# Kernel tuning notes

Hardware: AMD Instinct MI355X
Metric: run time of the kernel (lower is better)

The kernel has to match this reference:

```python
import jax, jax.numpy as jnp
import numpy as np

N = 50000          # num nodes
E = 600000         # num edges
F_IN = 128         # num_features
H = 128            # graph_hidden_dim
R = 2              # num_relations
L = 3              # n_layers_conv
BN_EPS = 1e-5
BN_BETA = 1e-4     # BatchNorm bias init per module code


def setup_inputs() -> dict:
    key = jax.random.key(0)
    ks = jax.random.split(key, 9)
    s_in = 1.0 / np.sqrt(F_IN)
    s_h = 1.0 / np.sqrt(H)
    return {
        "x": jax.random.normal(ks[0], (N, F_IN), jnp.float32),
        "edge_index": jax.random.randint(ks[1], (2, E), 0, N, jnp.int32),
        "edge_type": jax.random.randint(ks[2], (E,), 0, R, jnp.int32),
        "W0_rel": jax.random.normal(ks[3], (R, F_IN, H), jnp.float32) * s_in,
        "W0_root": jax.random.normal(ks[4], (F_IN, H), jnp.float32) * s_in,
        "b0": jnp.zeros((H,), jnp.float32),
        "Ws_rel": jax.random.normal(ks[5], (L, R, H, H), jnp.float32) * s_h,
        "Ws_root": jax.random.normal(ks[6], (L, H, H), jnp.float32) * s_h,
        "bs": jnp.zeros((L, H), jnp.float32),
    }


def batchnorm(x):
    # training-mode BatchNorm1d over nodes; weight=1, bias=1e-4 (per init)
    mu = jnp.mean(x, axis=0)
    var = jnp.mean((x - mu) ** 2, axis=0)  # biased var, as torch uses for norm
    return (x - mu) * jax.lax.rsqrt(var + BN_EPS) + BN_BETA


def rgcn_conv(x, src, dst, edge_type, W_rel, W_root, b):
    # PyG RGCNConv, aggr='mean': per-relation mean of x[src] at dst,
    # then per-relation linear, plus root transform and bias.
    seg = dst * R + edge_type  # combined (node, relation) segment id
    msgs = x[src]                                   # [E, d] gather
    sums = jax.ops.segment_sum(msgs, seg, num_segments=N * R)
    cnts = jax.ops.segment_sum(jnp.ones((src.shape[0],), x.dtype), seg,
                               num_segments=N * R)
    mean = sums.reshape(N, R, -1) / jnp.maximum(cnts, 1.0).reshape(N, R, 1)
    out = jnp.einsum('nrd,rdh->nh', mean, W_rel) + x @ W_root + b
    return out


def reference(x, edge_index, edge_type, W0_rel, W0_root, b0, Ws_rel, Ws_root, bs):
    src, dst = edge_index[0], edge_index[1]
    h = batchnorm(x)
    h = jax.nn.relu(rgcn_conv(h, src, dst, edge_type, W0_rel, W0_root, b0))
    for i in range(L):
        h_ = batchnorm(h)
        h_ = jax.nn.relu(rgcn_conv(h_, src, dst, edge_type,
                                   Ws_rel[i], Ws_root[i], bs[i]))
        h = h + h_  # conv_residual=True
    return h  # gconv_dropout == 0
```

## Files before the change

### kernel.cpp

```cpp
#include <hip/hip_runtime.h>
#include <hip/hip_bf16.h>

#define N_NODES 50000
#define N_EDGES 600000
#define F 128
#define R 2
#define NLAYER 4
#define NSEG (N_NODES * R)
#define SEGP (NSEG / 8)
#define NSCB 98
#define NB 384
#define BN_EPS 1e-5f
#define BETA 1e-4f

typedef __hip_bfloat16 bf16;
typedef __attribute__((ext_vector_type(8))) short short8;
typedef __attribute__((ext_vector_type(4))) float floatx4;

__global__ void k_wt(const float* __restrict__ W0_rel, const float* __restrict__ W0_root,
                     const float* __restrict__ Ws_rel, const float* __restrict__ Ws_root,
                     bf16* __restrict__ Bt) {
    int idx = blockIdx.x * 256 + threadIdx.x;
    if (idx >= NLAYER * NB * F) return;
    int l = idx / (NB * F);
    int rem = idx % (NB * F);
    int j = rem / F, d = rem % F;
    float v;
    if (j < 256) {
        int r = j >> 7, c = j & 127;
        v = (l == 0) ? W0_rel[(r * F + d) * F + c]
                     : Ws_rel[((size_t)((l - 1) * R + r) * F + d) * F + c];
    } else {
        int c = j - 256;
        v = (l == 0) ? W0_root[d * F + c]
                     : Ws_root[((size_t)(l - 1) * F + d) * F + c];
    }
    Bt[idx] = __float2bfloat16(v);
}

__global__ void k_count(const int* __restrict__ dst, const int* __restrict__ et,
                        int* __restrict__ cnt) {
    int g = blockIdx.x & 7;
    int lo = g * SEGP, hi = lo + SEGP;
    for (int e = (blockIdx.x >> 3) * 256 + threadIdx.x; e < N_EDGES; e += 65536) {
        int seg = dst[e] * R + et[e];
        if (seg >= lo && seg < hi) atomicAdd(&cnt[seg], 1);
    }
}

__global__ void k_scan1(const int* __restrict__ cnt, int* __restrict__ off,
                        int* __restrict__ bsum) {
    int t = threadIdx.x;
    int g = blockIdx.x * 1024 + t;
    int v = (g < NSEG) ? cnt[g] : 0;
    int lane = t & 63;
    int wv = t >> 6;
    int x = v;
    for (int d = 1; d < 64; d <<= 1) {
        int y = __shfl_up(x, d, 64);
        if (lane >= d) x += y;
    }
    __shared__ int wtot[16];
    if (lane == 63) wtot[wv] = x;
    __syncthreads();
    if (t < 16) {
        int s = wtot[t];
        for (int d = 1; d < 16; d <<= 1) {
            int y = __shfl_up(s, d, 64);
            if (t >= d) s += y;
        }
        wtot[t] = s;
    }
    __syncthreads();
    int wpre = (wv == 0) ? 0 : wtot[wv - 1];
    int incl = x + wpre;
    if (g < NSEG) off[g] = incl - v;
    if (t == 1023) bsum[blockIdx.x] = incl;
}

__global__ void k_scan2(int* __restrict__ bsum) {
    __shared__ int s[128];
    int t = threadIdx.x;
    int v = (t < NSCB) ? bsum[t] : 0;
    s[t] = v;
    __syncthreads();
    for (int d = 1; d < 128; d <<= 1) {
        int y = (t >= d) ? s[t - d] : 0;
        __syncthreads();
        s[t] += y;
        __syncthreads();
    }
    if (t < NSCB) bsum[t] = s[t] - v;
}

__global__ void k_scan3(int* __restrict__ off, const int* __restrict__ bsum) {
    int g = blockIdx.x * 1024 + threadIdx.x;
    if (g < NSEG) off[g] += bsum[blockIdx.x];
}

__global__ void k_fill(const int* __restrict__ src, const int* __restrict__ dst,
                       const int* __restrict__ et, const int* __restrict__ off,
                       int* __restrict__ fill, int* __restrict__ esrc) {
    int g = blockIdx.x & 7;
    int lo = g * SEGP, hi = lo + SEGP;
    for (int e = (blockIdx.x >> 3) * 256 + threadIdx.x; e < N_EDGES; e += 65536) {
        int seg = dst[e] * R + et[e];
        if (seg >= lo && seg < hi) {
            int idx = off[seg] + atomicAdd(&fill[seg], 1);
            esrc[idx] = src[e];
        }
    }
}

__global__ void k_bnstats(const float* __restrict__ h, float* __restrict__ gs) {
    int c = threadIdx.x & 127;
    int rl = threadIdx.x >> 7;
    float s = 0.f, q = 0.f;
    for (int r = blockIdx.x * 2 + rl; r < N_NODES; r += gridDim.x * 2) {
        float v = h[(size_t)r * F + c];
        s += v; q += v * v;
    }
    __shared__ float ls[256], lq[256];
    ls[threadIdx.x] = s; lq[threadIdx.x] = q;
    __syncthreads();
    if (rl == 0) {
        atomicAdd(&gs[c], ls[c] + ls[c + 128]);
        atomicAdd(&gs[128 + c], lq[c] + lq[c + 128]);
    }
}

__launch_bounds__(512)
__global__ void k_gemm(const float* __restrict__ h, const float* __restrict__ gs,
                       const bf16* __restrict__ Bt, const float* __restrict__ bias,
                       bf16* __restrict__ y, float* __restrict__ z) {
    __shared__ bf16 As[64 * 136];
    __shared__ bf16 Bs[128 * 136];
    int t = threadIdx.x;
    int m0 = blockIdx.x * 64;
    int c4 = (t & 31) * 4;
    float mu[4], rs[4];
    for (int c = 0; c < 4; c++) {
        float mm = gs[c4 + c] * (1.0f / N_NODES);
        float qq = gs[128 + c4 + c] * (1.0f / N_NODES);
        mu[c] = mm;
        rs[c] = rsqrtf(qq - mm * mm + BN_EPS);
    }
    int r0 = t >> 5;
    for (int it = 0; it < 4; it++) {
        int row = r0 + it * 16;
        int m = m0 + row;
        float4 v = {0.f, 0.f, 0.f, 0.f};
        if (m < N_NODES) v = *(const float4*)(h + (size_t)m * F + c4);
        bf16 o[4];
        o[0] = __float2bfloat16((v.x - mu[0]) * rs[0] + BETA);
        o[1] = __float2bfloat16((v.y - mu[1]) * rs[1] + BETA);
        o[2] = __float2bfloat16((v.z - mu[2]) * rs[2] + BETA);
        o[3] = __float2bfloat16((v.w - mu[3]) * rs[3] + BETA);
        *(double*)(As + row * 136 + c4) = *(const double*)o;
    }
    __syncthreads();
    int w = t >> 6;
    int lane = t & 63;
    int msub = w & 3;
    int nh = w >> 2;
    int lm = lane & 15;
    int lq = lane >> 4;
    short8 a[4];
    for (int ki = 0; ki < 4; ki++)
        a[ki] = *(const short8*)(As + (msub * 16 + lm) * 136 + ki * 32 + lq * 8);
    int m = m0 + msub * 16 + lm;
    for (int ci = 0; ci < 3; ci++) {
        __syncthreads();
        {
            const bf16* bsrc = Bt + (size_t)ci * 128 * F;
            for (int rr = 0; rr < 4; rr++) {
                int idx = rr * 512 + t;
                int row = idx >> 4;
                int kc = idx & 15;
                short8 v = *(const short8*)(bsrc + row * F + kc * 8);
                *(short8*)(Bs + row * 136 + kc * 8) = v;
            }
        }
        __syncthreads();
        for (int tt = 0; tt < 4; tt++) {
            int nt = nh * 4 + tt;
            short8 b[4];
            for (int ki = 0; ki < 4; ki++)
                b[ki] = *(const short8*)(Bs + (nt * 16 + lm) * 136 + ki * 32 + lq * 8);
            floatx4 acc = {0.f, 0.f, 0.f, 0.f};
            for (int ki = 0; ki < 4; ki++)
                acc = __builtin_amdgcn_mfma_f32_16x16x32_bf16(b[ki], a[ki], acc, 0, 0, 0);
            int n0 = ci * 128 + nt * 16 + lq * 4;
            if (m < N_NODES) {
                if (ci < 2) {
                    union { bf16 o[4]; double d; } u;
                    u.o[0] = __float2bfloat16(acc[0]);
                    u.o[1] = __float2bfloat16(acc[1]);
                    u.o[2] = __float2bfloat16(acc[2]);
                    u.o[3] = __float2bfloat16(acc[3]);
                    *(double*)(y + (size_t)m * 256 + n0) = u.d;
                } else {
                    float4 bv = *(const float4*)(bias + (n0 - 256));
                    float4 o4;
                    o4.x = acc[0] + bv.x;
                    o4.y = acc[1] + bv.y;
                    o4.z = acc[2] + bv.z;
                    o4.w = acc[3] + bv.w;
                    *(float4*)(z + (size_t)m * F + (n0 - 256)) = o4;
                }
            }
        }
    }
}

__global__ void k_aggregate(const bf16* __restrict__ y, const float* __restrict__ z,
                            const int* __restrict__ cnt, const int* __restrict__ off,
                            const int* __restrict__ esrc,
                            float* __restrict__ h, float* __restrict__ outp, int layer) {
    int wid = (blockIdx.x * 256 + threadIdx.x) >> 6;
    int lane = threadIdx.x & 63;
    if (wid >= N_NODES) return;
    int n = wid;
    int f = lane * 2;
    int2 cc = *(const int2*)(cnt + n * R);
    int c0 = cc.x, c1 = cc.y;
    int o0 = off[n * R];
    int ctot = c0 + c1;
    float inv0 = (c0 > 0) ? 1.0f / (float)c0 : 0.f;
    float inv1 = (c1 > 0) ? 1.0f / (float)c1 : 0.f;
    const bf16* yb = y + f;
    float2 zz = *(const float2*)(z + (size_t)n * F + f);
    float2 hp; hp.x = 0.f; hp.y = 0.f;
    if (layer > 0) hp = *(const float2*)(h + (size_t)n * F + f);
    float sa[8], sb[8];
    #pragma unroll
    for (int k = 0; k < 8; k++) { sa[k] = 0.f; sb[k] = 0.f; }
    int i = 0;
    for (; i + 8 <= ctot; i += 8) {
        int sn[8];
        #pragma unroll
        for (int k = 0; k < 8; k++) sn[k] = esrc[o0 + i + k];
        __hip_bfloat162 p[8];
        #pragma unroll
        for (int k = 0; k < 8; k++) {
            int ro = (i + k >= c0) ? 128 : 0;
            p[k] = *(const __hip_bfloat162*)(yb + (size_t)sn[k] * 256 + ro);
        }
        #pragma unroll
        for (int k = 0; k < 8; k++) {
            float wk = (i + k >= c0) ? inv1 : inv0;
            sa[k] = fmaf(__bfloat162float(p[k].x), wk, sa[k]);
            sb[k] = fmaf(__bfloat162float(p[k].y), wk, sb[k]);
        }
    }
    if (i + 4 <= ctot) {
        int sn[4];
        #pragma unroll
        for (int k = 0; k < 4; k++) sn[k] = esrc[o0 + i + k];
        __hip_bfloat162 p[4];
        #pragma unroll
        for (int k = 0; k < 4; k++) {
            int ro = (i + k >= c0) ? 128 : 0;
            p[k] = *(const __hip_bfloat162*)(yb + (size_t)sn[k] * 256 + ro);
        }
        #pragma unroll
        for (int k = 0; k < 4; k++) {
            float wk = (i + k >= c0) ? inv1 : inv0;
            sa[k] = fmaf(__bfloat162float(p[k].x), wk, sa[k]);
            sb[k] = fmaf(__bfloat162float(p[k].y), wk, sb[k]);
        }
        i += 4;
    }
    for (; i < ctot; i++) {
        int sn = esrc[o0 + i];
        int ro = (i >= c0) ? 128 : 0;
        float wk = (i >= c0) ? inv1 : inv0;
        __hip_bfloat162 p = *(const __hip_bfloat162*)(yb + (size_t)sn * 256 + ro);
        sa[0] = fmaf(__bfloat162float(p.x), wk, sa[0]);
        sb[0] = fmaf(__bfloat162float(p.y), wk, sb[0]);
    }
    float a0 = zz.x + (((sa[0] + sa[1]) + (sa[2] + sa[3])) + ((sa[4] + sa[5]) + (sa[6] + sa[7])));
    float a1 = zz.y + (((sb[0] + sb[1]) + (sb[2] + sb[3])) + ((sb[4] + sb[5]) + (sb[6] + sb[7])));
    a0 = fmaxf(a0, 0.f);
    a1 = fmaxf(a1, 0.f);
    a0 += hp.x;
    a1 += hp.y;
    float2 o2; o2.x = a0; o2.y = a1;
    *(float2*)(h + (size_t)n * F + f) = o2;
    if (outp) {
        float2 q2; q2.x = a0; q2.y = a1;
        *(float2*)(outp + (size_t)n * F + f) = q2;
    }
}

extern "C" void kernel_launch(void* const* d_in, const int* in_sizes, int n_in,
                              void* d_out, int out_size, void* d_ws, size_t ws_size,
                              hipStream_t stream) {
    const float* x       = (const float*)d_in[0];
    const int*   eidx    = (const int*)d_in[1];
    const int*   etype   = (const int*)d_in[2];
    const float* W0_rel  = (const float*)d_in[3];
    const float* W0_root = (const float*)d_in[4];
    const float* b0      = (const float*)d_in[5];
    const float* Ws_rel  = (const float*)d_in[6];
    const float* Ws_root = (const float*)d_in[7];
    const float* bs      = (const float*)d_in[8];
    const int* src = eidx;
    const int* dst = eidx + N_EDGES;

    char* w = (char*)d_ws;
    float* h   = (float*)w; w += (size_t)N_NODES * F * 4;
    float* z   = (float*)w; w += (size_t)N_NODES * F * 4;
    bf16*  y   = (bf16*)w;  w += (size_t)N_NODES * 256 * 2;
    bf16*  Bt  = (bf16*)w;  w += (size_t)NLAYER * NB * F * 2;
    int* cnt   = (int*)w;   w += (size_t)NSEG * 4;
    int* fill  = (int*)w;   w += (size_t)NSEG * 4;
    float* stats = (float*)w; w += (size_t)NLAYER * 256 * 4;
    int* off   = (int*)w;   w += (size_t)NSEG * 4;
    int* esrc  = (int*)w;   w += (size_t)N_EDGES * 4;
    int* bsum  = (int*)w;   w += 128 * 4;

    hipMemsetAsync(cnt, 0, (size_t)NSEG * 4 * 2 + (size_t)NLAYER * 256 * 4, stream);
    k_wt<<<(NLAYER * NB * F + 255) / 256, 256, 0, stream>>>(W0_rel, W0_root, Ws_rel, Ws_root, Bt);
    k_count<<<2048, 256, 0, stream>>>(dst, etype, cnt);
    k_scan1<<<NSCB, 1024, 0, stream>>>(cnt, off, bsum);
    k_scan2<<<1, 128, 0, stream>>>(bsum);
    k_scan3<<<NSCB, 1024, 0, stream>>>(off, bsum);
    k_fill<<<2048, 256, 0, stream>>>(src, dst, etype, off, fill, esrc);

    for (int l = 0; l < NLAYER; l++) {
        float* gs = stats + l * 256;
        const float* bias = (l == 0) ? b0 : (bs + (size_t)(l - 1) * F);
        const float* hin = (l == 0) ? x : h;
        k_bnstats<<<512, 256, 0, stream>>>(hin, gs);
        k_gemm<<<(N_NODES + 63) / 64, 512, 0, stream>>>(
            hin, gs, Bt + (size_t)l * NB * F, bias, y, z);
        k_aggregate<<<(N_NODES * 64 + 255) / 256, 256, 0, stream>>>(
            y, z, cnt, off, esrc, h, (l == 3) ? (float*)d_out : nullptr, l);
    }
}
```

Before: 488.2 us.

## Fuse next-layer BatchNorm statistics into aggregation and precompute segment ids

The aggregation kernel becomes a grid-stride loop over a fixed number of blocks. It accumulates per-feature sums and sums of squares of its outputs, which removes the separate BN stats pass over h for layers 1-3. The last layer now writes straight to the output instead of writing twice. Segment ids are computed once into a buffer that both count and fill reuse. The cost is reduced parallelism in the aggregation kernel (2048 blocks instead of about 12500) and contention on atomics at the end of each block.

```diff
diff --git a/kernel.cpp b/kernel.cpp
--- a/kernel.cpp
+++ b/kernel.cpp
@@ -10,6 +10,7 @@
 #define SEGP (NSEG / 8)
 #define NSCB 98
 #define NB 384
+#define AGG_BLOCKS 2048
 #define BN_EPS 1e-5f
 #define BETA 1e-4f
 
@@ -38,13 +39,18 @@
     Bt[idx] = __float2bfloat16(v);
 }
 
-__global__ void k_count(const int* __restrict__ dst, const int* __restrict__ et,
-                        int* __restrict__ cnt) {
+__global__ void k_seg(const int* __restrict__ dst, const int* __restrict__ et,
+                      int* __restrict__ seg) {
+    int e = blockIdx.x * 256 + threadIdx.x;
+    if (e < N_EDGES) seg[e] = dst[e] * R + et[e];
+}
+
+__global__ void k_count(const int* __restrict__ seg, int* __restrict__ cnt) {
     int g = blockIdx.x & 7;
     int lo = g * SEGP, hi = lo + SEGP;
     for (int e = (blockIdx.x >> 3) * 256 + threadIdx.x; e < N_EDGES; e += 65536) {
-        int seg = dst[e] * R + et[e];
-        if (seg >= lo && seg < hi) atomicAdd(&cnt[seg], 1);
+        int s = seg[e];
+        if (s >= lo && s < hi) atomicAdd(&cnt[s], 1);
     }
 }
 
@@ -98,15 +104,15 @@
     if (g < NSEG) off[g] += bsum[blockIdx.x];
 }
 
-__global__ void k_fill(const int* __restrict__ src, const int* __restrict__ dst,
-                       const int* __restrict__ et, const int* __restrict__ off,
+__global__ void k_fill(const int* __restrict__ src, const int* __restrict__ seg,
+                       const int* __restrict__ off,
                        int* __restrict__ fill, int* __restrict__ esrc) {
     int g = blockIdx.x & 7;
     int lo = g * SEGP, hi = lo + SEGP;
     for (int e = (blockIdx.x >> 3) * 256 + threadIdx.x; e < N_EDGES; e += 65536) {
-        int seg = dst[e] * R + et[e];
-        if (seg >= lo && seg < hi) {
-            int idx = off[seg] + atomicAdd(&fill[seg], 1);
+        int s = seg[e];
+        if (s >= lo && s < hi) {
+            int idx = off[s] + atomicAdd(&fill[s], 1);
             esrc[idx] = src[e];
         }
     }
@@ -216,80 +222,99 @@
 __global__ void k_aggregate(const bf16* __restrict__ y, const float* __restrict__ z,
                             const int* __restrict__ cnt, const int* __restrict__ off,
                             const int* __restrict__ esrc,
-                            float* __restrict__ h, float* __restrict__ outp, int layer) {
+                            const float* __restrict__ hres, float* __restrict__ hout,
+                            float* __restrict__ gs_next, int layer) {
     int wid = (blockIdx.x * 256 + threadIdx.x) >> 6;
     int lane = threadIdx.x & 63;
-    if (wid >= N_NODES) return;
-    int n = wid;
     int f = lane * 2;
-    int2 cc = *(const int2*)(cnt + n * R);
-    int c0 = cc.x, c1 = cc.y;
-    int o0 = off[n * R];
-    int ctot = c0 + c1;
-    float inv0 = (c0 > 0) ? 1.0f / (float)c0 : 0.f;
-    float inv1 = (c1 > 0) ? 1.0f / (float)c1 : 0.f;
+    float s0 = 0.f, s1 = 0.f, q0 = 0.f, q1 = 0.f;
     const bf16* yb = y + f;
-    float2 zz = *(const float2*)(z + (size_t)n * F + f);
-    float2 hp; hp.x = 0.f; hp.y = 0.f;
-    if (layer > 0) hp = *(const float2*)(h + (size_t)n * F + f);
-    float sa[8], sb[8];
-    #pragma unroll
-    for (int k = 0; k < 8; k++) { sa[k] = 0.f; sb[k] = 0.f; }
-    int i = 0;
-    for (; i + 8 <= ctot; i += 8) {
-        int sn[8];
+    for (int n = wid; n < N_NODES; n += AGG_BLOCKS * 4) {
+        int2 cc = *(const int2*)(cnt + n * R);
+        int c0 = cc.x, c1 = cc.y;
+        int o0 = off[n * R];
+        int ctot = c0 + c1;
+        float inv0 = (c0 > 0) ? 1.0f / (float)c0 : 0.f;
+        float inv1 = (c1 > 0) ? 1.0f / (float)c1 : 0.f;
+        float2 zz = *(const float2*)(z + (size_t)n * F + f);
+        float2 hp; hp.x = 0.f; hp.y = 0.f;
+        if (layer > 0) hp = *(const float2*)(hres + (size_t)n * F + f);
+        float sa[8], sb[8];
         #pragma unroll
-        for (int k = 0; k < 8; k++) sn[k] = esrc[o0 + i + k];
-        __hip_bfloat162 p[8];
-        #pragma unroll
-        for (int k = 0; k < 8; k++) {
-            int ro = (i + k >= c0) ? 128 : 0;
-            p[k] = *(const __hip_bfloat162*)(yb + (size_t)sn[k] * 256 + ro);
-        }
-        #pragma unroll
-        for (int k = 0; k < 8; k++) {
-            float wk = (i + k >= c0) ? inv1 : inv0;
-            sa[k] = fmaf(__bfloat162float(p[k].x), wk, sa[k]);
-            sb[k] = fmaf(__bfloat162float(p[k].y), wk, sb[k]);
-        }
-    }
-    if (i + 4 <= ctot) {
-        int sn[4];
-        #pragma unroll
-        for (int k = 0; k < 4; k++) sn[k] = esrc[o0 + i + k];
-        __hip_bfloat162 p[4];
-        #pragma unroll
-        for (int k = 0; k < 4; k++) {
-            int ro = (i + k >= c0) ? 128 : 0;
-            p[k] = *(const __hip_bfloat162*)(yb + (size_t)sn[k] * 256 + ro);
-        }
-        #pragma unroll
-        for (int k = 0; k < 4; k++) {
-            float wk = (i + k >= c0) ? inv1 : inv0;
-            sa[k] = fmaf(__bfloat162float(p[k].x), wk, sa[k]);
-            sb[k] = fmaf(__bfloat162float(p[k].y), wk, sb[k]);
-        }
-        i += 4;
-    }
-    for (; i < ctot; i++) {
-        int sn = esrc[o0 + i];
-        int ro = (i >= c0) ? 128 : 0;
-        float wk = (i >= c0) ? inv1 : inv0;
-        __hip_bfloat162 p = *(const __hip_bfloat162*)(yb + (size_t)sn * 256 + ro);
-        sa[0] = fmaf(__bfloat162float(p.x), wk, sa[0]);
-        sb[0] = fmaf(__bfloat162float(p.y), wk, sb[0]);
-    }
-    float a0 = zz.x + (((sa[0] + sa[1]) + (sa[2] + sa[3])) + ((sa[4] + sa[5]) + (sa[6] + sa[7])));
-    float a1 = zz.y + (((sb[0] + sb[1]) + (sb[2] + sb[3])) + ((sb[4] + sb[5]) + (sb[6] + sb[7])));
-    a0 = fmaxf(a0, 0.f);
-    a1 = fmaxf(a1, 0.f);
-    a0 += hp.x;
-    a1 += hp.y;
-    float2 o2; o2.x = a0; o2.y = a1;
-    *(float2*)(h + (size_t)n * F + f) = o2;
-    if (outp) {
-        float2 q2; q2.x = a0; q2.y = a1;
-        *(float2*)(outp + (size_t)n * F + f) = q2;
+        for (int k = 0; k < 8; k++) { sa[k] = 0.f; sb[k] = 0.f; }
+        int i = 0;
+        for (; i + 8 <= ctot; i += 8) {
+            int sn[8];
+            #pragma unroll
+            for (int k = 0; k < 8; k++) sn[k] = esrc[o0 + i + k];
+            __hip_bfloat162 p[8];
+            #pragma unroll
+            for (int k = 0; k < 8; k++) {
+                int ro = (i + k >= c0) ? 128 : 0;
+                p[k] = *(const __hip_bfloat162*)(yb + (size_t)sn[k] * 256 + ro);
+            }
+            #pragma unroll
+            for (int k = 0; k < 8; k++) {
+                float wk = (i + k >= c0) ? inv1 : inv0;
+                sa[k] = fmaf(__bfloat162float(p[k].x), wk, sa[k]);
+                sb[k] = fmaf(__bfloat162float(p[k].y), wk, sb[k]);
+            }
+        }
+        if (i + 4 <= ctot) {
+            int sn[4];
+            #pragma unroll
+            for (int k = 0; k < 4; k++) sn[k] = esrc[o0 + i + k];
+            __hip_bfloat162 p[4];
+            #pragma unroll
+            for (int k = 0; k < 4; k++) {
+                int ro = (i + k >= c0) ? 128 : 0;
+                p[k] = *(const __hip_bfloat162*)(yb + (size_t)sn[k] * 256 + ro);
+            }
+            #pragma unroll
+            for (int k = 0; k < 4; k++) {
+                float wk = (i + k >= c0) ? inv1 : inv0;
+                sa[k] = fmaf(__bfloat162float(p[k].x), wk, sa[k]);
+                sb[k] = fmaf(__bfloat162float(p[k].y), wk, sb[k]);
+            }
+            i += 4;
+        }
+        for (; i < ctot; i++) {
+            int sn = esrc[o0 + i];
+            int ro = (i >= c0) ? 128 : 0;
+            float wk = (i >= c0) ? inv1 : inv0;
+            __hip_bfloat162 p = *(const __hip_bfloat162*)(yb + (size_t)sn * 256 + ro);
+            sa[0] = fmaf(__bfloat162float(p.x), wk, sa[0]);
+            sb[0] = fmaf(__bfloat162float(p.y), wk, sb[0]);
+        }
+        float a0 = zz.x + (((sa[0] + sa[1]) + (sa[2] + sa[3])) + ((sa[4] + sa[5]) + (sa[6] + sa[7])));
+        float a1 = zz.y + (((sb[0] + sb[1]) + (sb[2] + sb[3])) + ((sb[4] + sb[5]) + (sb[6] + sb[7])));
+        a0 = fmaxf(a0, 0.f);
+        a1 = fmaxf(a1, 0.f);
+        a0 += hp.x;
+        a1 += hp.y;
+        float2 o2; o2.x = a0; o2.y = a1;
+        *(float2*)(hout + (size_t)n * F + f) = o2;
+        if (gs_next) {
+            s0 += a0; s1 += a1;
+            q0 = fmaf(a0, a0, q0); q1 = fmaf(a1, a1, q1);
+        }
+    }
+    if (gs_next) {
+        __shared__ float rs_[4 * 128];
+        __shared__ float rq_[4 * 128];
+        int w = threadIdx.x >> 6;
+        rs_[w * 128 + f] = s0; rs_[w * 128 + f + 1] = s1;
+        rq_[w * 128 + f] = q0; rq_[w * 128 + f + 1] = q1;
+        __syncthreads();
+        int t = threadIdx.x;
+        if (t < 128) {
+            float S = (rs_[t] + rs_[128 + t]) + (rs_[256 + t] + rs_[384 + t]);
+            atomicAdd(&gs_next[t], S);
+        } else {
+            int c = t - 128;
+            float Q = (rq_[c] + rq_[128 + c]) + (rq_[256 + c] + rq_[384 + c]);
+            atomicAdd(&gs_next[128 + c], Q);
+        }
     }
 }
 
@@ -318,24 +343,27 @@
     float* stats = (float*)w; w += (size_t)NLAYER * 256 * 4;
     int* off   = (int*)w;   w += (size_t)NSEG * 4;
     int* esrc  = (int*)w;   w += (size_t)N_EDGES * 4;
+    int* segb  = (int*)w;   w += (size_t)N_EDGES * 4;
     int* bsum  = (int*)w;   w += 128 * 4;
 
     hipMemsetAsync(cnt, 0, (size_t)NSEG * 4 * 2 + (size_t)NLAYER * 256 * 4, stream);
     k_wt<<<(NLAYER * NB * F + 255) / 256, 256, 0, stream>>>(W0_rel, W0_root, Ws_rel, Ws_root, Bt);
-    k_count<<<2048, 256, 0, stream>>>(dst, etype, cnt);
+    k_seg<<<(N_EDGES + 255) / 256, 256, 0, stream>>>(dst, etype, segb);
+    k_count<<<2048, 256, 0, stream>>>(segb, cnt);
     k_scan1<<<NSCB, 1024, 0, stream>>>(cnt, off, bsum);
     k_scan2<<<1, 128, 0, stream>>>(bsum);
     k_scan3<<<NSCB, 1024, 0, stream>>>(off, bsum);
-    k_fill<<<2048, 256, 0, stream>>>(src, dst, etype, off, fill, esrc);
+    k_fill<<<2048, 256, 0, stream>>>(src, segb, off, fill, esrc);
+    k_bnstats<<<512, 256, 0, stream>>>(x, stats);
 
     for (int l = 0; l < NLAYER; l++) {
         float* gs = stats + l * 256;
         const float* bias = (l == 0) ? b0 : (bs + (size_t)(l - 1) * F);
         const float* hin = (l == 0) ? x : h;
-        k_bnstats<<<512, 256, 0, stream>>>(hin, gs);
         k_gemm<<<(N_NODES + 63) / 64, 512, 0, stream>>>(
             hin, gs, Bt + (size_t)l * NB * F, bias, y, z);
-        k_aggregate<<<(N_NODES * 64 + 255) / 256, 256, 0, stream>>>(
-            y, z, cnt, off, esrc, h, (l == 3) ? (float*)d_out : nullptr, l);
-    }
-}
+        k_aggregate<<<AGG_BLOCKS, 256, 0, stream>>>(
+            y, z, cnt, off, esrc, h, (l == 3) ? (float*)d_out : h,
+            (l < 3) ? (stats + (l + 1) * 256) : nullptr, l);
+    }
+}
```

After: 577.7 us. 1.18x slower.
